# Kernel optimization log

Measured on AMD Instinct MI355X. Metric: run time of the kernel, lower is better.

The kernel has to match this reference:

```python
import jax, jax.numpy as jnp
import numpy as np

VOCAB = 30000; PAD = 0; H = 128; ROOT = 128; MAX_NODES = 1024; NUM_REL = 64
NL = MAX_NODES // ROOT - 1   # 7 leaves per root node (num_leaves)
LH = 4                       # head span length (all head_lengths == LH)
B = 64


def setup_inputs():
    key = jax.random.key(0)
    ks = jax.random.split(key, 6)
    # tokens >= 1 so no pad tokens: every leaf is populated -> all tail spans have length NL
    input_nodes = jax.random.randint(ks[0], (B, MAX_NODES, 1), 1, VOCAB, dtype=jnp.int32)
    leaf_relationships = jax.random.randint(ks[1], (B, ROOT), 1, NUM_REL + 1, dtype=jnp.int32)
    head_lengths = jnp.full((B, ROOT), LH, dtype=jnp.int32)
    atom_emb = (jax.random.normal(ks[2], (VOCAB, H), jnp.float32) * 0.02).at[PAD].set(0.0)
    rel_mat_emb = (jax.random.normal(ks[3], (NUM_REL + 1, H * H), jnp.float32) * 0.05).at[0].set(0.0)
    rel_emb = (jax.random.normal(ks[4], (NUM_REL + 1, 2 * H), jnp.float32) * 0.05).at[0].set(0.0)
    graph_token = jax.random.normal(ks[5], (1, H), jnp.float32) * 0.02
    return {"input_nodes": input_nodes, "leaf_relationships": leaf_relationships,
            "head_lengths": head_lengths, "atom_emb": atom_emb,
            "rel_mat_emb": rel_mat_emb, "rel_emb": rel_emb, "graph_token": graph_token}


def reference(input_nodes, leaf_relationships, head_lengths, atom_emb, rel_mat_emb, rel_emb, graph_token):
    Bq, N, F = input_nodes.shape          # F == 1 (required by original code's squeeze(1))
    node_feature = atom_emb[input_nodes].sum(axis=-2)   # [B,N,H], sum over atom-feature dim
    tok = input_nodes[..., 0]                           # [B,N]

    # head spans: one span per root node, start = root index, length LH, clamped like torch
    r_idx = jnp.arange(ROOT)
    head_pos = jnp.clip(r_idx[:, None] + jnp.arange(LH)[None, :], 0, ROOT - 1)   # [ROOT,LH]
    # tail spans: contiguous leaves per root, fixed length NL
    tail_pos = ROOT + r_idx[:, None] * NL + jnp.arange(NL)[None, :]              # [ROOT,NL]
    head_tok = tok[:, head_pos].reshape(Bq * ROOT, LH)
    tail_tok = tok[:, tail_pos].reshape(Bq * ROOT, NL)

    # triples ordered row-major over (batch, root) exactly like torch.nonzero
    rels = leaf_relationships.reshape(-1)                # [S], S = B*ROOT
    M = rel_mat_emb[rels].reshape(-1, H, H)              # [S,H,H] relation matrices (dropout is eval/identity)
    r = rel_emb[rels]                                    # [S,2H]
    he = atom_emb[head_tok]                              # [S,LH,H]
    te = atom_emb[tail_tok]                              # [S,NL,H]

    Mt = jnp.einsum('sij,stj->sti', M, te)               # M @ tail_embed per tail
    Mh = jnp.einsum('sij,shj->shi', M, he)               # M @ head_embed per head
    # torch views bmm output [H,2] as [2H] -> interleaved (Mt, Mh); r dotted with it:
    a = jnp.einsum('si,sti->st', r[:, 0::2], Mt)
    b = jnp.einsum('si,shi->sh', r[:, 1::2], Mh)
    scores = jax.nn.leaky_relu(a[:, :, None] + b[:, None, :], negative_slope=0.01)  # [S,NL,LH]
    alpha = jax.nn.softmax(scores, axis=-1)              # softmax over heads (dim=0 of [LH] in torch)
    hsum = jnp.einsum('sth,shj->stj', alpha, he)         # head_embed @ alphas
    final = jnp.einsum('sij,stj->sti', M, hsum)          # [S,NL,H]

    # scatter-add: destination node for triple (b,r), tail t is ROOT + r*NL + t -> contiguous leaf block
    node_feature = node_feature.at[:, ROOT:].add(final.reshape(Bq, ROOT * NL, H))
    gt = jnp.broadcast_to(graph_token[None], (Bq, 1, H))
    return jnp.concatenate([gt, node_feature], axis=1)   # [B, N+1, H]
```

## Files before the change

kernel.cpp:

```cpp
#include <hip/hip_runtime.h>
#include <hip/hip_bf16.h>
#include <stdint.h>

typedef unsigned int u32;

#define BATCH 64
#define ROOT 128
#define NLEAF 7
#define LHEAD 4
#define HDIM 128
#define NNODES 1024
#define OUTROWS 1025
#define NREL1 65
#define PSTR 132

typedef __attribute__((ext_vector_type(8))) short bf16x8;
typedef __attribute__((ext_vector_type(4))) float f32x4;

__device__ float g_U[NREL1 * HDIM];
__device__ float g_V[NREL1 * HDIM];
__device__ u32   g_Mfrag[NREL1 * 8192];

static __device__ __forceinline__ u32 rne_bf16(float f) {
    u32 u = __builtin_bit_cast(u32, f);
    return (u + 0x7fffu + ((u >> 16) & 1u)) >> 16;
}
static __device__ __forceinline__ u32 pack_bf16(float a, float b) {
    return rne_bf16(a) | (rne_bf16(b) << 16);
}

__global__ void prep_kernel(const float* __restrict__ rel_mat,
                            const float* __restrict__ rel_emb) {
    int rel = blockIdx.x;
    int part = blockIdx.y;
    const float* M = rel_mat + (size_t)rel * HDIM * HDIM;
    __shared__ float red_u[8][32], red_v[8][32];

    if (part < 4) {
        u32* dst = &g_Mfrag[(size_t)rel * 8192];
        #pragma unroll
        for (int q = 0; q < 8; ++q) {
            int o = part * 2048 + q * 256 + threadIdx.x;
            int r  = o >> 10;
            int t  = (o >> 8) & 3;
            int ln = (o >> 2) & 63;
            int dw = o & 3;
            int i = r * 16 + (ln & 15);
            int j = t * 32 + ((ln >> 4) << 3) + dw * 2;
            dst[o] = pack_bf16(M[i * HDIM + j], M[i * HDIM + j + 1]);
        }
    } else {
        int p = part - 4;
        int jj = threadIdx.x & 31, s = threadIdx.x >> 5;
        int j = p * 32 + jj;
        const float* r = rel_emb + (size_t)rel * 2 * HDIM;
        float u = 0.f, v = 0.f;
        #pragma unroll
        for (int ii = 0; ii < 16; ++ii) {
            int i = s * 16 + ii;
            float m = M[i * HDIM + j];
            u += r[2 * i] * m;
            v += r[2 * i + 1] * m;
        }
        red_u[s][jj] = u; red_v[s][jj] = v;
        __syncthreads();
        if (s == 0) {
            float su = 0.f, sv = 0.f;
            #pragma unroll
            for (int q = 0; q < 8; ++q) { su += red_u[q][jj]; sv += red_v[q][jj]; }
            g_U[rel * HDIM + j] = su;
            g_V[rel * HDIM + j] = sv;
        }
    }
}

__global__ __launch_bounds__(256) void triple_kernel(
    const int* __restrict__ tok,
    const int* __restrict__ leaf_rel,
    const float* __restrict__ atom,
    const float* __restrict__ gtok,
    float* __restrict__ out)
{
    int g = blockIdx.x;
    int b = blockIdx.y;
    int tid = threadIdx.x;
    int wave = tid >> 6, lane = tid & 63;
    int rn = g * 4 + wave;

    __shared__ __align__(16) float he_s[4][LHEAD][PSTR];
    __shared__ __align__(16) float MhT[4][LHEAD][PSTR];

    int rel = leaf_rel[b * ROOT + rn];

    int tokidx = 0;
    if (lane < LHEAD + NLEAF) {
        int pos;
        if (lane < LHEAD) { int hp = rn + lane; if (hp > ROOT - 1) hp = ROOT - 1; pos = hp; }
        else              pos = ROOT + rn * NLEAF + (lane - LHEAD);
        tokidx = tok[b * NNODES + pos];
    }
    int htok[LHEAD], ttok[NLEAF];
    #pragma unroll
    for (int l = 0; l < LHEAD; ++l) htok[l] = __shfl(tokidx, l, 64);
    #pragma unroll
    for (int t = 0; t < NLEAF; ++t) ttok[t] = __shfl(tokidx, LHEAD + t, 64);

    float he_lo[LHEAD], he_hi[LHEAD], te_lo[NLEAF], te_hi[NLEAF];
    #pragma unroll
    for (int l = 0; l < LHEAD; ++l) {
        const float* r = atom + (size_t)htok[l] * HDIM;
        he_lo[l] = r[lane]; he_hi[l] = r[lane + 64];
    }
    #pragma unroll
    for (int t = 0; t < NLEAF; ++t) {
        const float* r = atom + (size_t)ttok[t] * HDIM;
        te_lo[t] = r[lane]; te_hi[t] = r[lane + 64];
    }

    const float* U = &g_U[rel * HDIM];
    const float* V = &g_V[rel * HDIM];
    float u_lo = U[lane], u_hi = U[lane + 64];
    float v_lo = V[lane], v_hi = V[lane + 64];

    #pragma unroll
    for (int l = 0; l < LHEAD; ++l) {
        he_s[wave][l][lane]      = he_lo[l];
        he_s[wave][l][lane + 64] = he_hi[l];
    }

    float a_r[NLEAF], b_r[LHEAD];
    #pragma unroll
    for (int t = 0; t < NLEAF; ++t) {
        float p = u_lo * te_lo[t] + u_hi * te_hi[t];
        #pragma unroll
        for (int m = 32; m > 0; m >>= 1) p += __shfl_xor(p, m, 64);
        a_r[t] = p;
    }
    #pragma unroll
    for (int l = 0; l < LHEAD; ++l) {
        float p = v_lo * he_lo[l] + v_hi * he_hi[l];
        #pragma unroll
        for (int m = 32; m > 0; m >>= 1) p += __shfl_xor(p, m, 64);
        b_r[l] = p;
    }

    int nn = lane & 15;
    int kb = (lane >> 4) << 3;
    uint4 bfr[4];
    #pragma unroll
    for (int t = 0; t < 4; ++t) {
        const float* h = &he_s[wave][nn & 3][t * 32 + kb];
        float4 f0 = *(const float4*)h;
        float4 f1 = *(const float4*)(h + 4);
        bfr[t].x = pack_bf16(f0.x, f0.y);
        bfr[t].y = pack_bf16(f0.z, f0.w);
        bfr[t].z = pack_bf16(f1.x, f1.y);
        bfr[t].w = pack_bf16(f1.z, f1.w);
    }

    const uint4* Mf = ((const uint4*)g_Mfrag) + (size_t)rel * 2048;
    #pragma unroll
    for (int rt = 0; rt < 8; ++rt) {
        f32x4 acc = {0.f, 0.f, 0.f, 0.f};
        #pragma unroll
        for (int kt = 0; kt < 4; ++kt) {
            uint4 afr = Mf[(rt * 4 + kt) * 64 + lane];
            acc = __builtin_amdgcn_mfma_f32_16x16x32_bf16(
                      __builtin_bit_cast(bf16x8, afr),
                      __builtin_bit_cast(bf16x8, bfr[kt]), acc, 0, 0, 0);
        }
        if (nn < LHEAD) {
            int row0 = rt * 16 + ((lane >> 4) << 2);
            *(float4*)&MhT[wave][nn][row0] = make_float4(acc[0], acc[1], acc[2], acc[3]);
        }
    }

    size_t bbase = (size_t)b * OUTROWS * HDIM;
    out[bbase + (size_t)(1 + rn) * HDIM + lane]      = he_lo[0];
    out[bbase + (size_t)(1 + rn) * HDIM + lane + 64] = he_hi[0];
    if (g == 0 && wave == 0) {
        out[bbase + lane]      = gtok[lane];
        out[bbase + lane + 64] = gtok[lane + 64];
    }

    size_t obase = bbase + (size_t)(1 + ROOT + rn * NLEAF) * HDIM;
    #pragma unroll
    for (int t = 0; t < NLEAF; ++t) {
        float sc[LHEAD]; float mx = -1e30f;
        #pragma unroll
        for (int l = 0; l < LHEAD; ++l) {
            float x = a_r[t] + b_r[l];
            x = (x >= 0.f) ? x : 0.01f * x;
            sc[l] = x; mx = fmaxf(mx, x);
        }
        float sum = 0.f;
        #pragma unroll
        for (int l = 0; l < LHEAD; ++l) { sc[l] = __expf(sc[l] - mx); sum += sc[l]; }
        float inv = 1.f / sum;
        float r0 = te_lo[t], r1 = te_hi[t];
        #pragma unroll
        for (int l = 0; l < LHEAD; ++l) {
            float al = sc[l] * inv;
            r0 += al * MhT[wave][l][lane];
            r1 += al * MhT[wave][l][lane + 64];
        }
        out[obase + t * HDIM + lane]      = r0;
        out[obase + t * HDIM + lane + 64] = r1;
    }
}

extern "C" void kernel_launch(void* const* d_in, const int* in_sizes, int n_in,
                              void* d_out, int out_size, void* d_ws, size_t ws_size,
                              hipStream_t stream) {
    (void)in_sizes; (void)n_in; (void)out_size; (void)d_ws; (void)ws_size;
    const int* tok       = (const int*)d_in[0];
    const int* leaf_rel  = (const int*)d_in[1];
    const float* atom    = (const float*)d_in[3];
    const float* rel_mat = (const float*)d_in[4];
    const float* rel_emb = (const float*)d_in[5];
    const float* gtok    = (const float*)d_in[6];
    float* out = (float*)d_out;

    dim3 pgrid(NREL1, 8);
    prep_kernel<<<pgrid, 256, 0, stream>>>(rel_mat, rel_emb);

    dim3 grid(ROOT / 4, BATCH);
    triple_kernel<<<grid, 256, 0, stream>>>(tok, leaf_rel, atom, gtok, out);
}
```

Measured before the change: 111.8 us.

## Compute attention scores from the MFMA output instead of precomputed U/V projections

Head and tail embeddings are now loaded straight into the MFMA B fragments, filling 11 of the 16 columns instead of 4. The scores a and b are then formed as dot products of the M-multiplied vectors with the even and odd halves of rel_emb, reduced with shuffles. This removes the prep kernel's U/V matrix-vector reduction, the he_s shared-memory staging, and the 11 full-wave shuffle reductions. The trade-off is that scores are now computed from bf16-rounded products rather than fp32, which adds rounding error, and each lane issues more scattered global loads for the B fragments.

```diff
diff --git a/kernel.cpp b/kernel.cpp
--- a/kernel.cpp
+++ b/kernel.cpp
@@ -17,9 +17,9 @@
 typedef __attribute__((ext_vector_type(8))) short bf16x8;
 typedef __attribute__((ext_vector_type(4))) float f32x4;
 
-__device__ float g_U[NREL1 * HDIM];
-__device__ float g_V[NREL1 * HDIM];
 __device__ u32   g_Mfrag[NREL1 * 8192];
+__device__ float g_Re[NREL1 * HDIM];
+__device__ float g_Ro[NREL1 * HDIM];
 
 static __device__ __forceinline__ u32 rne_bf16(float f) {
     u32 u = __builtin_bit_cast(u32, f);
@@ -34,7 +34,6 @@
     int rel = blockIdx.x;
     int part = blockIdx.y;
     const float* M = rel_mat + (size_t)rel * HDIM * HDIM;
-    __shared__ float red_u[8][32], red_v[8][32];
 
     if (part < 4) {
         u32* dst = &g_Mfrag[(size_t)rel * 8192];
@@ -50,27 +49,10 @@
             dst[o] = pack_bf16(M[i * HDIM + j], M[i * HDIM + j + 1]);
         }
     } else {
-        int p = part - 4;
-        int jj = threadIdx.x & 31, s = threadIdx.x >> 5;
-        int j = p * 32 + jj;
-        const float* r = rel_emb + (size_t)rel * 2 * HDIM;
-        float u = 0.f, v = 0.f;
-        #pragma unroll
-        for (int ii = 0; ii < 16; ++ii) {
-            int i = s * 16 + ii;
-            float m = M[i * HDIM + j];
-            u += r[2 * i] * m;
-            v += r[2 * i + 1] * m;
-        }
-        red_u[s][jj] = u; red_v[s][jj] = v;
-        __syncthreads();
-        if (s == 0) {
-            float su = 0.f, sv = 0.f;
-            #pragma unroll
-            for (int q = 0; q < 8; ++q) { su += red_u[q][jj]; sv += red_v[q][jj]; }
-            g_U[rel * HDIM + j] = su;
-            g_V[rel * HDIM + j] = sv;
-        }
+        int i = threadIdx.x;
+        float v = rel_emb[(size_t)rel * 2 * HDIM + i];
+        if (i & 1) g_Ro[rel * HDIM + (i >> 1)] = v;
+        else       g_Re[rel * HDIM + (i >> 1)] = v;
     }
 }
 
@@ -87,7 +69,6 @@
     int wave = tid >> 6, lane = tid & 63;
     int rn = g * 4 + wave;
 
-    __shared__ __align__(16) float he_s[4][LHEAD][PSTR];
     __shared__ __align__(16) float MhT[4][LHEAD][PSTR];
 
     int rel = leaf_rel[b * ROOT + rn];
@@ -99,66 +80,42 @@
         else              pos = ROOT + rn * NLEAF + (lane - LHEAD);
         tokidx = tok[b * NNODES + pos];
     }
-    int htok[LHEAD], ttok[NLEAF];
-    #pragma unroll
-    for (int l = 0; l < LHEAD; ++l) htok[l] = __shfl(tokidx, l, 64);
-    #pragma unroll
-    for (int t = 0; t < NLEAF; ++t) ttok[t] = __shfl(tokidx, LHEAD + t, 64);
-
-    float he_lo[LHEAD], he_hi[LHEAD], te_lo[NLEAF], te_hi[NLEAF];
-    #pragma unroll
-    for (int l = 0; l < LHEAD; ++l) {
-        const float* r = atom + (size_t)htok[l] * HDIM;
-        he_lo[l] = r[lane]; he_hi[l] = r[lane + 64];
-    }
-    #pragma unroll
-    for (int t = 0; t < NLEAF; ++t) {
-        const float* r = atom + (size_t)ttok[t] * HDIM;
-        te_lo[t] = r[lane]; te_hi[t] = r[lane + 64];
-    }
-
-    const float* U = &g_U[rel * HDIM];
-    const float* V = &g_V[rel * HDIM];
-    float u_lo = U[lane], u_hi = U[lane + 64];
-    float v_lo = V[lane], v_hi = V[lane + 64];
-
-    #pragma unroll
-    for (int l = 0; l < LHEAD; ++l) {
-        he_s[wave][l][lane]      = he_lo[l];
-        he_s[wave][l][lane + 64] = he_hi[l];
-    }
-
-    float a_r[NLEAF], b_r[LHEAD];
-    #pragma unroll
-    for (int t = 0; t < NLEAF; ++t) {
-        float p = u_lo * te_lo[t] + u_hi * te_hi[t];
-        #pragma unroll
-        for (int m = 32; m > 0; m >>= 1) p += __shfl_xor(p, m, 64);
-        a_r[t] = p;
-    }
-    #pragma unroll
-    for (int l = 0; l < LHEAD; ++l) {
-        float p = v_lo * he_lo[l] + v_hi * he_hi[l];
-        #pragma unroll
-        for (int m = 32; m > 0; m >>= 1) p += __shfl_xor(p, m, 64);
-        b_r[l] = p;
-    }
 
     int nn = lane & 15;
     int kb = (lane >> 4) << 3;
+    int sel = (nn < LHEAD + NLEAF) ? nn : 0;
+    int tokrow = __shfl(tokidx, sel, 64);
+
+    float te_lo[NLEAF], te_hi[NLEAF];
+    #pragma unroll
+    for (int t = 0; t < NLEAF; ++t) {
+        int tt = __shfl(tokidx, LHEAD + t, 64);
+        const float* r = atom + (size_t)tt * HDIM;
+        te_lo[t] = r[lane]; te_hi[t] = r[lane + 64];
+    }
+    int h0 = __shfl(tokidx, 0, 64);
+    const float* hr = atom + (size_t)h0 * HDIM;
+    float he0_lo = hr[lane], he0_hi = hr[lane + 64];
+
+    const float* arow = atom + (size_t)tokrow * HDIM + kb;
     uint4 bfr[4];
     #pragma unroll
-    for (int t = 0; t < 4; ++t) {
-        const float* h = &he_s[wave][nn & 3][t * 32 + kb];
-        float4 f0 = *(const float4*)h;
-        float4 f1 = *(const float4*)(h + 4);
-        bfr[t].x = pack_bf16(f0.x, f0.y);
-        bfr[t].y = pack_bf16(f0.z, f0.w);
-        bfr[t].z = pack_bf16(f1.x, f1.y);
-        bfr[t].w = pack_bf16(f1.z, f1.w);
+    for (int kt = 0; kt < 4; ++kt) {
+        float4 f0 = *(const float4*)(arow + kt * 32);
+        float4 f1 = *(const float4*)(arow + kt * 32 + 4);
+        bfr[kt].x = pack_bf16(f0.x, f0.y);
+        bfr[kt].y = pack_bf16(f0.z, f0.w);
+        bfr[kt].z = pack_bf16(f1.x, f1.y);
+        bfr[kt].w = pack_bf16(f1.z, f1.w);
     }
 
+    const float* rbase = ((nn < LHEAD) ? g_Ro : g_Re) + rel * HDIM + ((lane >> 4) << 2);
+    float4 rreg[8];
+    #pragma unroll
+    for (int rt = 0; rt < 8; ++rt) rreg[rt] = *(const float4*)(rbase + rt * 16);
+
     const uint4* Mf = ((const uint4*)g_Mfrag) + (size_t)rel * 2048;
+    float dp = 0.f;
     #pragma unroll
     for (int rt = 0; rt < 8; ++rt) {
         f32x4 acc = {0.f, 0.f, 0.f, 0.f};
@@ -169,15 +126,26 @@
                       __builtin_bit_cast(bf16x8, afr),
                       __builtin_bit_cast(bf16x8, bfr[kt]), acc, 0, 0, 0);
         }
+        dp += rreg[rt].x * acc[0] + rreg[rt].y * acc[1]
+            + rreg[rt].z * acc[2] + rreg[rt].w * acc[3];
         if (nn < LHEAD) {
             int row0 = rt * 16 + ((lane >> 4) << 2);
             *(float4*)&MhT[wave][nn][row0] = make_float4(acc[0], acc[1], acc[2], acc[3]);
         }
     }
 
+    dp += __shfl_xor(dp, 16, 64);
+    dp += __shfl_xor(dp, 32, 64);
+
+    float b_r[LHEAD], a_r[NLEAF];
+    #pragma unroll
+    for (int l = 0; l < LHEAD; ++l) b_r[l] = __shfl(dp, l, 64);
+    #pragma unroll
+    for (int t = 0; t < NLEAF; ++t) a_r[t] = __shfl(dp, LHEAD + t, 64);
+
     size_t bbase = (size_t)b * OUTROWS * HDIM;
-    out[bbase + (size_t)(1 + rn) * HDIM + lane]      = he_lo[0];
-    out[bbase + (size_t)(1 + rn) * HDIM + lane + 64] = he_hi[0];
+    out[bbase + (size_t)(1 + rn) * HDIM + lane]      = he0_lo;
+    out[bbase + (size_t)(1 + rn) * HDIM + lane + 64] = he0_hi;
     if (g == 0 && wave == 0) {
         out[bbase + lane]      = gtok[lane];
         out[bbase + lane + 64] = gtok[lane + 64];
@@ -221,7 +189,7 @@
     const float* gtok    = (const float*)d_in[6];
     float* out = (float*)d_out;
 
-    dim3 pgrid(NREL1, 8);
+    dim3 pgrid(NREL1, 5);
     prep_kernel<<<pgrid, 256, 0, stream>>>(rel_mat, rel_emb);
 
     dim3 grid(ROOT / 4, BATCH);
```

Result: no change. 111.7 us (-0.0%).
